# Kernel optimization log

Hardware: AMD Instinct MI355X
Metric: run time of the kernel (lower is better)

The kernel has to match this reference:

```python
import jax, jax.numpy as jnp
import numpy as np
from jax import lax

B, T, C, H, K = 2, 4096, 2048, 16, 4
D = C // H
EPS = 1e-5


def _ln(x, g, b):
    m = x.mean(-1, keepdims=True)
    v = ((x - m) ** 2).mean(-1, keepdims=True)
    return (x - m) / jnp.sqrt(v + EPS) * g + b


def _l2norm(x):
    n = jnp.sqrt(jnp.sum(x * x, axis=-1, keepdims=True))
    return x / jnp.maximum(n, 1e-12)


def setup_inputs() -> dict:
    key = jax.random.key(0)
    ks = jax.random.split(key, 10)
    s = 1.0 / np.sqrt(C)
    x = jax.random.normal(ks[0], (B, T, C), jnp.float32)
    Wq = jax.random.normal(ks[1], (C, C), jnp.float32) * s
    Wk = jax.random.normal(ks[2], (C, C), jnp.float32) * s
    Wv = jax.random.normal(ks[3], (C, C), jnp.float32) * s
    Wo = jax.random.normal(ks[4], (C, C), jnp.float32) * s
    conv_w = jax.random.normal(ks[5], (C, 1, K), jnp.float32) * 0.5  # depthwise (O, I/g, K)
    conv_b = jnp.zeros((C,), jnp.float32)
    Wig = jax.random.normal(ks[6], (C, C), jnp.float32) * 0.02
    big = jnp.full((C,), -2.0, jnp.float32)  # gate_init_bias
    Wog = jax.random.normal(ks[7], (C, C), jnp.float32) * s
    bog = jnp.zeros((C,), jnp.float32)
    Wgam = jax.random.normal(ks[8], (H, C), jnp.float32) * 0.02
    decays = 1.0 - np.exp(np.linspace(np.log(1 - 0.9), np.log(1 - 0.9999), H))
    bgam = jnp.asarray(np.log(decays / (1 - decays)), jnp.float32)
    vn_g = jnp.ones((D,), jnp.float32); vn_b = jnp.zeros((D,), jnp.float32)
    mn_g = jnp.ones((D,), jnp.float32); mn_b = jnp.zeros((D,), jnp.float32)
    gn_g = jnp.ones((C,), jnp.float32); gn_b = jnp.zeros((C,), jnp.float32)
    return dict(x=x, Wq=Wq, Wk=Wk, Wv=Wv, Wo=Wo, conv_w=conv_w, conv_b=conv_b,
                Wig=Wig, big=big, Wog=Wog, bog=bog, Wgam=Wgam, bgam=bgam,
                vn_g=vn_g, vn_b=vn_b, mn_g=mn_g, mn_b=mn_b, gn_g=gn_g, gn_b=gn_b)


def reference(x, Wq, Wk, Wv, Wo, conv_w, conv_b, Wig, big, Wog, bog, Wgam, bgam,
              vn_g, vn_b, mn_g, mn_b, gn_g, gn_b):
    # Causal depthwise conv1d over time
    xt = jnp.transpose(x, (0, 2, 1))                     # [B,C,T]
    xp = jnp.pad(xt, ((0, 0), (0, 0), (K - 1, 0)))
    xc = lax.conv_general_dilated(xp, conv_w, (1,), 'VALID', feature_group_count=C)
    xc = xc + conv_b[None, :, None]
    x_conv = jax.nn.silu(jnp.transpose(xc, (0, 2, 1)))   # [B,T,C]

    q = _l2norm((x @ Wq.T).reshape(B, T, H, D))
    k = _l2norm((x @ Wk.T).reshape(B, T, H, D))
    v = _ln((x @ Wv.T).reshape(B, T, H, D), vn_g, vn_b)
    i_gate = jax.nn.sigmoid(x_conv @ Wig.T + big).reshape(B, T, H, D)
    gamma = jax.nn.sigmoid(x_conv @ Wgam.T + bgam).reshape(B, T, H, 1)

    # Gated linear recurrence: mem_t = gamma_t * mem_{t-1} + i_t * k_t * v_t
    kv = i_gate * k * v
    def combine(c1, c2):
        a1, b1 = c1
        a2, b2 = c2
        return a1 * a2, a2 * b1 + b2
    _, mem = lax.associative_scan(combine, (gamma, kv), axis=1)  # mem: [B,T,H,D]

    mem_out = _ln(mem, mn_g, mn_b)
    out = (mem_out * q).reshape(B * T, H, D)
    # GroupNorm(num_groups=H) over channels
    m = out.mean(-1, keepdims=True)
    var = ((out - m) ** 2).mean(-1, keepdims=True)
    out = (out - m) / jnp.sqrt(var + EPS)
    out = out * gn_g.reshape(H, D) + gn_b.reshape(H, D)
    out = out.reshape(B, T, C)
    out = out * jax.nn.sigmoid(x_conv @ Wog.T + bog)
    return out @ Wo.T
```

## Files before the change

### kernel.cpp

```cpp
#include <hip/hip_runtime.h>
#include <cstdint>
#include <cstddef>

using u16 = unsigned short;
using bf16x8 = __attribute__((ext_vector_type(8))) __bf16;
using f32x4  = __attribute__((ext_vector_type(4))) float;

constexpr int Bb = 2, Tt = 4096, Cc = 2048, Hh = 16, Dd = 128;
constexpr int Mm = Bb * Tt;
constexpr int CHK = 32;
constexpr int NCH = Tt / CHK;
constexpr float EPSf = 1e-5f;

__device__ __forceinline__ u16 f2bf(float f) {
  union { float f; uint32_t u; } v; v.f = f;
  return (u16)((v.u + 0x7fffu + ((v.u >> 16) & 1u)) >> 16);
}
__device__ __forceinline__ float bf2f(u16 h) {
  union { uint32_t u; float f; } v; v.u = ((uint32_t)h) << 16;
  return v.f;
}
__device__ __forceinline__ float sig_(float z) { return 1.f / (1.f + __expf(-z)); }
__device__ __forceinline__ float wred(float v) {
#pragma unroll
  for (int m = 32; m; m >>= 1) v += __shfl_xor(v, m);
  return v;
}
__device__ __forceinline__ void glds16(const u16* g, u16* l) {
  __builtin_amdgcn_global_load_lds(
      (const __attribute__((address_space(1))) unsigned int*)g,
      (__attribute__((address_space(3))) unsigned int*)l, 16, 0, 0);
}

__global__ void la_conv(const float* __restrict__ x, const float* __restrict__ cw,
                        const float* __restrict__ cb, u16* __restrict__ xbf,
                        u16* __restrict__ xconv) {
  int i4 = blockIdx.x * 256 + threadIdx.x;
  int c4 = i4 & (Cc / 4 - 1);
  int bt = i4 >> 9;
  int t = bt & (Tt - 1);
  const float4* x4 = (const float4*)x;
  float4 xv = x4[i4];
  float4 xm1 = t >= 1 ? x4[i4 - Cc / 4] : make_float4(0, 0, 0, 0);
  float4 xm2 = t >= 2 ? x4[i4 - Cc / 2] : make_float4(0, 0, 0, 0);
  float4 xm3 = t >= 3 ? x4[i4 - 3 * Cc / 4] : make_float4(0, 0, 0, 0);
  ushort4 ob; ushort4 oc;
  const float4* cw4 = (const float4*)cw;
  float vv[4]  = {xv.x, xv.y, xv.z, xv.w};
  float v1[4]  = {xm1.x, xm1.y, xm1.z, xm1.w};
  float v2[4]  = {xm2.x, xm2.y, xm2.z, xm2.w};
  float v3[4]  = {xm3.x, xm3.y, xm3.z, xm3.w};
  u16 rb[4], rc[4];
#pragma unroll
  for (int j = 0; j < 4; j++) {
    int c = c4 * 4 + j;
    float4 w = cw4[c];
    float acc = cb[c] + w.w * vv[j] + w.z * v1[j] + w.y * v2[j] + w.x * v3[j];
    rb[j] = f2bf(vv[j]);
    rc[j] = f2bf(acc * sig_(acc));
  }
  ob.x = rb[0]; ob.y = rb[1]; ob.z = rb[2]; ob.w = rb[3];
  oc.x = rc[0]; oc.y = rc[1]; oc.z = rc[2]; oc.w = rc[3];
  ((ushort4*)xbf)[i4] = ob;
  ((ushort4*)xconv)[i4] = oc;
}

__global__ void la_cvt5(const float* w0, const float* w1, const float* w2,
                        const float* w3, const float* w4,
                        u16* o0, u16* o1, u16* o2, u16* o3, u16* o4, int n4each) {
  int i = blockIdx.x * 256 + threadIdx.x;
  int seg = i / n4each;
  int off = i - seg * n4each;
  const float* src = seg == 0 ? w0 : seg == 1 ? w1 : seg == 2 ? w2 : seg == 3 ? w3 : w4;
  u16* dst = seg == 0 ? o0 : seg == 1 ? o1 : seg == 2 ? o2 : seg == 3 ? o3 : o4;
  float4 v = ((const float4*)src)[off];
  ushort4 o;
  o.x = f2bf(v.x); o.y = f2bf(v.y); o.z = f2bf(v.z); o.w = f2bf(v.w);
  ((ushort4*)dst)[off] = o;
}

__global__ void la_cvt(const float* __restrict__ in, u16* __restrict__ out, int n4) {
  int i = blockIdx.x * 256 + threadIdx.x;
  if (i < n4) {
    float4 v = ((const float4*)in)[i];
    ushort4 o;
    o.x = f2bf(v.x); o.y = f2bf(v.y); o.z = f2bf(v.z); o.w = f2bf(v.w);
    ((ushort4*)out)[i] = o;
  }
}

__global__ __launch_bounds__(256) void la_gamma(
    const u16* __restrict__ xconv, const float* __restrict__ Wg,
    const float* __restrict__ bg, float* __restrict__ gam) {
  __shared__ u16 wlds[Hh * Cc];
  for (int i = threadIdx.x; i < Hh * Cc / 4; i += 256) {
    float4 v = ((const float4*)Wg)[i];
    ushort4 o;
    o.x = f2bf(v.x); o.y = f2bf(v.y); o.z = f2bf(v.z); o.w = f2bf(v.w);
    ((ushort4*)wlds)[i] = o;
  }
  __syncthreads();
  const int wave = threadIdx.x >> 6, lane = threadIdx.x & 63;
  const int row0 = blockIdx.x * 16 + wave * 4;
#pragma unroll
  for (int r = 0; r < 4; r++) {
    const int row = row0 + r;
    const u16* xr = xconv + (size_t)row * Cc + lane * 8;
    bf16x8 xv[4];
#pragma unroll
    for (int it = 0; it < 4; it++) xv[it] = *(const bf16x8*)(xr + it * 512);
#pragma unroll
    for (int h = 0; h < 16; h++) {
      const u16* wr = wlds + h * Cc + lane * 8;
      float acc = 0.f;
#pragma unroll
      for (int it = 0; it < 4; it++) {
        bf16x8 wv = *(const bf16x8*)(wr + it * 512);
#pragma unroll
        for (int e = 0; e < 8; e++) acc += (float)xv[it][e] * (float)wv[e];
      }
      acc = wred(acc);
      if (lane == 0) gam[row * Hh + h] = sig_(acc + bg[h]);
    }
  }
}

__global__ void la_prep(const u16* pq, const u16* pk, const u16* pv, const u16* pig,
                        const float* __restrict__ vng, const float* __restrict__ vnb,
                        const float* __restrict__ bigv, u16* qo, u16* kvo) {
  const int wave = threadIdx.x >> 6, lane = threadIdx.x & 63;
  const int p = blockIdx.x * 4 + wave;
  const int row = p >> 4, h = p & 15;
  const int d0 = lane * 2;
  const size_t base = (size_t)row * Cc + h * Dd + d0;
  uint32_t uq = *(const uint32_t*)(pq + base);
  uint32_t uk = *(const uint32_t*)(pk + base);
  uint32_t uv = *(const uint32_t*)(pv + base);
  uint32_t ui = *(const uint32_t*)(pig + base);
  float q0 = bf2f((u16)uq), q1 = bf2f((u16)(uq >> 16));
  float k0 = bf2f((u16)uk), k1 = bf2f((u16)(uk >> 16));
  float v0 = bf2f((u16)uv), v1 = bf2f((u16)(uv >> 16));
  float i0 = bf2f((u16)ui), i1 = bf2f((u16)(ui >> 16));
  float qs = wred(q0*q0 + q1*q1);
  float ks = wred(k0*k0 + k1*k1);
  float s1 = wred(v0 + v1);
  float s2 = wred(v0*v0 + v1*v1);
  float qn = 1.f / fmaxf(sqrtf(qs), 1e-12f);
  float kn = 1.f / fmaxf(sqrtf(ks), 1e-12f);
  float mu = s1 * (1.f / Dd);
  float var = s2 * (1.f / Dd) - mu * mu;
  float rs = rsqrtf(var + EPSf);
  int c0 = h * Dd + d0;
  float vh0 = (v0 - mu) * rs * vng[d0]     + vnb[d0];
  float vh1 = (v1 - mu) * rs * vng[d0 + 1] + vnb[d0 + 1];
  float ig0 = sig_(i0 + bigv[c0]);
  float ig1 = sig_(i1 + bigv[c0 + 1]);
  float kv0 = ig0 * (k0 * kn) * vh0;
  float kv1 = ig1 * (k1 * kn) * vh1;
  *(uint32_t*)(qo + base)  = (uint32_t)f2bf(q0 * qn) | ((uint32_t)f2bf(q1 * qn) << 16);
  *(uint32_t*)(kvo + base) = (uint32_t)f2bf(kv0)     | ((uint32_t)f2bf(kv1) << 16);
}

__global__ void la_scan1(u16* __restrict__ kv, float* __restrict__ gam,
                         float* __restrict__ Ebuf) {
  const int wave = threadIdx.x >> 6, lane = threadIdx.x & 63;
  const int p = blockIdx.x * 4 + wave;
  const int bh = p >> 7, c = p & (NCH - 1);
  const int b = bh >> 4, h = bh & 15;
  const int t0 = c * CHK;
  const size_t rbase = (size_t)b * Tt + t0;
  const size_t base = rbase * Cc + h * Dd + lane * 2;
  float* gp = gam + rbase * Hh + h;
  float m0 = 0.f, m1 = 0.f, cg = 1.f;
#pragma unroll 4
  for (int t = 0; t < CHK; t++) {
    float g = gp[(size_t)t * Hh];
    cg *= g;
    uint32_t u = *(const uint32_t*)(kv + base + (size_t)t * Cc);
    m0 = fmaf(g, m0, bf2f((u16)u));
    m1 = fmaf(g, m1, bf2f((u16)(u >> 16)));
    *(uint32_t*)(kv + base + (size_t)t * Cc) =
        (uint32_t)f2bf(m0) | ((uint32_t)f2bf(m1) << 16);
    if (lane == 0) gp[(size_t)t * Hh] = cg;
  }
  float2 e; e.x = m0; e.y = m1;
  *(float2*)&Ebuf[(size_t)p * Dd + lane * 2] = e;
}

__global__ void la_scan2(const float* __restrict__ Ebuf, const float* __restrict__ cumg,
                         float* __restrict__ carry) {
  const int bh = blockIdx.x;
  const int b = bh >> 4, h = bh & 15;
  const int lane = threadIdx.x;
  float S0 = 0.f, S1 = 0.f;
  for (int c = 0; c < NCH; c++) {
    size_t idx = ((size_t)bh * NCH + c) * Dd + lane * 2;
    float2 s; s.x = S0; s.y = S1;
    *(float2*)&carry[idx] = s;
    float2 E = *(const float2*)&Ebuf[idx];
    float P = cumg[((size_t)b * Tt + c * CHK + CHK - 1) * Hh + h];
    S0 = fmaf(P, S0, E.x);
    S1 = fmaf(P, S1, E.y);
  }
}

__global__ void la_post(const u16* mem, const u16* q, const u16* ogp,
                        const float* __restrict__ cumg, const float* __restrict__ carry,
                        const float* __restrict__ mng, const float* __restrict__ mnb,
                        const float* __restrict__ gng, const float* __restrict__ gnb,
                        const float* __restrict__ bog, u16* outb) {
  const int wave = threadIdx.x >> 6, lane = threadIdx.x & 63;
  const int p = blockIdx.x * 4 + wave;
  const int row = p >> 4, h = p & 15;
  const int b = row >> 12, t = row & (Tt - 1), ch = t >> 5;
  const int d0 = lane * 2;
  const size_t base = (size_t)row * Cc + h * Dd + d0;
  uint32_t um = *(const uint32_t*)(mem + base);
  uint32_t uq = *(const uint32_t*)(q + base);
  uint32_t uo = *(const uint32_t*)(ogp + base);
  float cg = cumg[p];
  float2 cr = *(const float2*)&carry[(((size_t)(b * Hh + h)) * NCH + ch) * Dd + d0];
  float m0 = fmaf(cg, cr.x, bf2f((u16)um));
  float m1 = fmaf(cg, cr.y, bf2f((u16)(um >> 16)));
  float q0 = bf2f((u16)uq), q1 = bf2f((u16)(uq >> 16));
  float g0 = bf2f((u16)uo), g1 = bf2f((u16)(uo >> 16));
  float s1 = wred(m0 + m1);
  float s2 = wred(m0*m0 + m1*m1);
  float mu = s1 * (1.f / Dd);
  float var = s2 * (1.f / Dd) - mu * mu;
  float rs = rsqrtf(var + EPSf);
  int c0 = h * Dd + d0;
  float mo0 = (m0 - mu) * rs * mng[d0]     + mnb[d0];
  float mo1 = (m1 - mu) * rs * mng[d0 + 1] + mnb[d0 + 1];
  float o0 = mo0 * q0, o1 = mo1 * q1;
  float t1 = wred(o0 + o1);
  float t2 = wred(o0*o0 + o1*o1);
  float mu2 = t1 * (1.f / Dd);
  float var2 = t2 * (1.f / Dd) - mu2 * mu2;
  float rs2 = rsqrtf(var2 + EPSf);
  float y0 = (o0 - mu2) * rs2 * gng[c0]     + gnb[c0];
  float y1 = (o1 - mu2) * rs2 * gng[c0 + 1] + gnb[c0 + 1];
  y0 *= sig_(g0 + bog[c0]);
  y1 *= sig_(g1 + bog[c0 + 1]);
  *(uint32_t*)(outb + base) = (uint32_t)f2bf(y0) | ((uint32_t)f2bf(y1) << 16);
}

template <int OUT_BF16>
__global__ __launch_bounds__(256)
void la_gemm(const u16* __restrict__ A,
             const u16* __restrict__ W0, const u16* __restrict__ W1,
             const u16* __restrict__ W2,
             void* __restrict__ C0, void* __restrict__ C1, void* __restrict__ C2,
             int K) {
  __shared__ u16 As[128 * 64];
  __shared__ u16 Bs[128 * 64];
  const int tid = threadIdx.x;
  const int lane = tid & 63;
  const int wave = tid >> 6;
  const int seg = blockIdx.x >> 4;
  const int bn = (blockIdx.x & 15) * 128;
  const int bm = blockIdx.y * 128;
  const u16* W = seg == 0 ? W0 : (seg == 1 ? W1 : W2);
  void* Co = seg == 0 ? C0 : (seg == 1 ? C1 : C2);
  const int wm = (wave >> 1) * 64;
  const int wn = (wave & 1) * 64;
  const int fm = lane & 15;

  const int srow = wave * 32 + (lane >> 3);
  const int sg   = ((lane & 7) ^ (lane >> 3)) * 8;
  const u16* Ag = A + (size_t)(bm + srow) * K + sg;
  const u16* Wg = W + (size_t)(bn + srow) * K + sg;
  u16* lA = As + wave * 2048;
  u16* lB = Bs + wave * 2048;

  f32x4 acc[4][4] = {};

  for (int k0 = 0; k0 < K; k0 += 64) {
#pragma unroll
    for (int j = 0; j < 4; j++) {
      glds16(Ag + k0 + j * 8 * K, lA + j * 512);
      glds16(Wg + k0 + j * 8 * K, lB + j * 512);
    }
    __syncthreads();
#pragma unroll
    for (int kk = 0; kk < 2; kk++) {
      const int qs = (((lane >> 4) + kk * 4) ^ (fm & 7)) * 8;
      bf16x8 af[4], bfr[4];
#pragma unroll
      for (int i = 0; i < 4; i++)
        af[i] = *(const bf16x8*)&As[(wm + i * 16 + fm) * 64 + qs];
#pragma unroll
      for (int j = 0; j < 4; j++)
        bfr[j] = *(const bf16x8*)&Bs[(wn + j * 16 + fm) * 64 + qs];
#pragma unroll
      for (int i = 0; i < 4; i++)
#pragma unroll
        for (int j = 0; j < 4; j++)
          acc[i][j] = __builtin_amdgcn_mfma_f32_16x16x32_bf16(af[i], bfr[j], acc[i][j], 0, 0, 0);
    }
    __syncthreads();
  }

  const int cr = (lane >> 4) * 4;
  const int cc = lane & 15;
#pragma unroll
  for (int i = 0; i < 4; i++) {
#pragma unroll
    for (int j = 0; j < 4; j++) {
#pragma unroll
      for (int r = 0; r < 4; r++) {
        size_t off = (size_t)(bm + wm + i * 16 + cr + r) * Cc + (bn + wn + j * 16 + cc);
        if (OUT_BF16) ((u16*)Co)[off] = f2bf(acc[i][j][r]);
        else          ((float*)Co)[off] = acc[i][j][r];
      }
    }
  }
}

extern "C" void kernel_launch(void* const* d_in, const int* in_sizes, int n_in,
                              void* d_out, int out_size, void* d_ws, size_t ws_size,
                              hipStream_t stream) {
  (void)in_sizes; (void)n_in; (void)out_size; (void)ws_size;
  const float* x    = (const float*)d_in[0];
  const float* Wq   = (const float*)d_in[1];
  const float* Wk   = (const float*)d_in[2];
  const float* Wv   = (const float*)d_in[3];
  const float* Wo   = (const float*)d_in[4];
  const float* cw   = (const float*)d_in[5];
  const float* cb   = (const float*)d_in[6];
  const float* Wig  = (const float*)d_in[7];
  const float* big  = (const float*)d_in[8];
  const float* Wog  = (const float*)d_in[9];
  const float* bog  = (const float*)d_in[10];
  const float* Wgam = (const float*)d_in[11];
  const float* bgam = (const float*)d_in[12];
  const float* vng  = (const float*)d_in[13];
  const float* vnb  = (const float*)d_in[14];
  const float* mng  = (const float*)d_in[15];
  const float* mnb  = (const float*)d_in[16];
  const float* gng  = (const float*)d_in[17];
  const float* gnb  = (const float*)d_in[18];

  char* ws = (char*)d_ws;
  const size_t NB = (size_t)Mm * Cc * 2;
  u16* xbf   = (u16*)(ws + 0 * NB);
  u16* xconv = (u16*)(ws + 1 * NB);
  u16* preq  = (u16*)(ws + 2 * NB);
  u16* prek  = (u16*)(ws + 3 * NB);
  u16* prev  = (u16*)(ws + 4 * NB);
  u16* preig = (u16*)(ws + 5 * NB);
  u16* wbf   = (u16*)(ws + 6 * NB);
  float* gam = (float*)(ws + 6 * NB + (size_t)Cc * Cc * 2);
  const size_t WE = (size_t)Cc * Cc;
  u16* wk_bf  = preig;
  u16* wv_bf  = preig + WE;
  u16* wig_bf = preig + 2 * WE;
  u16* wog_bf = preig + 3 * WE;
  float* Ebuf  = (float*)preig;
  float* carry = (float*)(preig + 1024 * 1024);
  u16* ogscr = (u16*)d_out;

  const int WN4 = Cc * Cc / 4;
  dim3 blk(256);

  la_conv<<<Mm * Cc / 4 / 256, blk, 0, stream>>>(x, cw, cb, xbf, xconv);

  la_cvt5<<<5 * WN4 / 256, blk, 0, stream>>>(Wq, Wk, Wv, Wig, Wog,
                                             wbf, wk_bf, wv_bf, wig_bf, wog_bf, WN4);

  la_gemm<1><<<dim3(48, Mm / 128), blk, 0, stream>>>(
      xbf, wbf, wk_bf, wv_bf, (void*)preq, (void*)prek, (void*)prev, Cc);

  la_cvt<<<WN4 / 256, blk, 0, stream>>>(Wo, wbf, WN4);

  la_gemm<1><<<dim3(32, Mm / 128), blk, 0, stream>>>(
      xconv, wig_bf, wog_bf, wog_bf, (void*)xbf, (void*)ogscr, (void*)ogscr, Cc);

  la_gamma<<<Mm / 16, blk, 0, stream>>>(xconv, Wgam, bgam, gam);

  la_prep<<<Mm * Hh / 4, blk, 0, stream>>>(preq, prek, prev, xbf,
                                           vng, vnb, big, preq, prek);

  la_scan1<<<Bb * Hh * NCH / 4, blk, 0, stream>>>(prek, gam, Ebuf);
  la_scan2<<<Bb * Hh, dim3(64), 0, stream>>>(Ebuf, gam, carry);

  la_post<<<Mm * Hh / 4, blk, 0, stream>>>(prek, preq, ogscr, gam, carry,
                                           mng, mnb, gng, gnb, bog, xbf);

  la_gemm<0><<<dim3(16, Mm / 128), blk, 0, stream>>>(
      xbf, wbf, wbf, wbf, d_out, d_out, d_out, Cc);
}
```

Measured before the change: 855.2 us.

## Rewrite bf16 GEMM as 256x256 tile with 8 waves and double-buffered LDS pipeline

Replaces the 128x128, 4-wave GEMM with a 256x256 tile computed by 8 waves. The tile is split into four 128-row/128-col sub-blocks, and global-to-LDS loads are staged two iterations ahead in a double-buffered 128KB LDS region, with raw s_barrier and explicit waitcnt interleaving loads and MFMAs. It raises per-block data reuse and hides memory latency behind MFMA work. The cost is a much larger LDS footprint and register pressure, and the hand-placed barriers and vmcnt counts are fragile.

```diff
diff --git a/kernel.cpp b/kernel.cpp
--- a/kernel.cpp
+++ b/kernel.cpp
@@ -31,6 +31,7 @@
       (const __attribute__((address_space(1))) unsigned int*)g,
       (__attribute__((address_space(3))) unsigned int*)l, 16, 0, 0);
 }
+__device__ __forceinline__ void bar_() { asm volatile("s_barrier" ::: "memory"); }
 
 __global__ void la_conv(const float* __restrict__ x, const float* __restrict__ cw,
                         const float* __restrict__ cb, u16* __restrict__ xbf,
@@ -245,76 +246,129 @@
   *(uint32_t*)(outb + base) = (uint32_t)f2bf(y0) | ((uint32_t)f2bf(y1) << 16);
 }
 
+#define STAGE(t, j) do {                                                        \
+    const u16* _s = (((j) == 0 || (j) == 2) ? Ab : Wb)                          \
+                    + (((j) == 1 || (j) == 2) ? (size_t)128 * K : (size_t)0)    \
+                    + soff + (size_t)(t) * 64;                                  \
+    u16* _d = dbase + ((((t) & 1) * 4 + (j)) * 8192);                           \
+    glds16(_s, _d);                                                             \
+    glds16(_s + 8 * (size_t)K, _d + 512);                                       \
+  } while (0)
+
+#define LDFRAG(DST, NFR, SLOT, RBASE) do {                                      \
+    _Pragma("unroll")                                                           \
+    for (int _i = 0; _i < (NFR); ++_i)                                          \
+      _Pragma("unroll")                                                         \
+      for (int _ks = 0; _ks < 2; ++_ks)                                         \
+        DST[_i][_ks] = *(const bf16x8*)&(SLOT)[((RBASE) + _i * 16) * 64 +       \
+                         ((((lane >> 4) + _ks * 4) ^ x7) * 8)];                 \
+  } while (0)
+
+#define MM16(QM, QN, BB) do {                                                   \
+    __builtin_amdgcn_s_setprio(1);                                             \
+    _Pragma("unroll")                                                           \
+    for (int _mi = 0; _mi < 4; ++_mi)                                           \
+      _Pragma("unroll")                                                         \
+      for (int _ni = 0; _ni < 2; ++_ni)                                         \
+        _Pragma("unroll")                                                       \
+        for (int _ks = 0; _ks < 2; ++_ks)                                       \
+          acc[QM][QN][_mi][_ni] = __builtin_amdgcn_mfma_f32_16x16x32_bf16(      \
+              a[_mi][_ks], BB[_ni][_ks], acc[QM][QN][_mi][_ni], 0, 0, 0);       \
+    __builtin_amdgcn_s_setprio(0);                                             \
+  } while (0)
+
 template <int OUT_BF16>
-__global__ __launch_bounds__(256)
+__global__ __launch_bounds__(512, 2)
 void la_gemm(const u16* __restrict__ A,
              const u16* __restrict__ W0, const u16* __restrict__ W1,
              const u16* __restrict__ W2,
              void* __restrict__ C0, void* __restrict__ C1, void* __restrict__ C2,
              int K) {
-  __shared__ u16 As[128 * 64];
-  __shared__ u16 Bs[128 * 64];
-  const int tid = threadIdx.x;
+  __shared__ u16 lds[8 * 8192];
+  const int tid  = threadIdx.x;
   const int lane = tid & 63;
-  const int wave = tid >> 6;
-  const int seg = blockIdx.x >> 4;
-  const int bn = (blockIdx.x & 15) * 128;
-  const int bm = blockIdx.y * 128;
+  const int wv   = tid >> 6;
+  const int wm = wv >> 2;
+  const int wn = wv & 3;
+  const int fm = lane & 15;
+  const int x7 = fm & 7;
+  const int seg = blockIdx.x >> 3;
+  const int bn = (blockIdx.x & 7) * 256;
+  const int bm = blockIdx.y * 256;
   const u16* W = seg == 0 ? W0 : (seg == 1 ? W1 : W2);
   void* Co = seg == 0 ? C0 : (seg == 1 ? C1 : C2);
-  const int wm = (wave >> 1) * 64;
-  const int wn = (wave & 1) * 64;
-  const int fm = lane & 15;
-
-  const int srow = wave * 32 + (lane >> 3);
-  const int sg   = ((lane & 7) ^ (lane >> 3)) * 8;
-  const u16* Ag = A + (size_t)(bm + srow) * K + sg;
-  const u16* Wg = W + (size_t)(bn + srow) * K + sg;
-  u16* lA = As + wave * 2048;
-  u16* lB = Bs + wave * 2048;
-
-  f32x4 acc[4][4] = {};
-
-  for (int k0 = 0; k0 < K; k0 += 64) {
-#pragma unroll
-    for (int j = 0; j < 4; j++) {
-      glds16(Ag + k0 + j * 8 * K, lA + j * 512);
-      glds16(Wg + k0 + j * 8 * K, lB + j * 512);
-    }
-    __syncthreads();
-#pragma unroll
-    for (int kk = 0; kk < 2; kk++) {
-      const int qs = (((lane >> 4) + kk * 4) ^ (fm & 7)) * 8;
-      bf16x8 af[4], bfr[4];
-#pragma unroll
-      for (int i = 0; i < 4; i++)
-        af[i] = *(const bf16x8*)&As[(wm + i * 16 + fm) * 64 + qs];
-#pragma unroll
-      for (int j = 0; j < 4; j++)
-        bfr[j] = *(const bf16x8*)&Bs[(wn + j * 16 + fm) * 64 + qs];
-#pragma unroll
-      for (int i = 0; i < 4; i++)
-#pragma unroll
-        for (int j = 0; j < 4; j++)
-          acc[i][j] = __builtin_amdgcn_mfma_f32_16x16x32_bf16(af[i], bfr[j], acc[i][j], 0, 0, 0);
-    }
-    __syncthreads();
+
+  const u16* Ab = A + (size_t)bm * K;
+  const u16* Wb = W + (size_t)bn * K;
+  const size_t soff = (size_t)(wv * 16 + (lane >> 3)) * K
+                      + (size_t)(((lane & 7) ^ (lane >> 3)) * 8);
+  u16* const dbase = lds + wv * 1024;
+  const int nkt = K >> 6;
+  const int ra = wm * 64 + fm;
+  const int rb = wn * 32 + fm;
+
+  f32x4 acc[2][2][4][2] = {};
+  bf16x8 a[4][2], b0[2][2], b1[2][2];
+
+  STAGE(0, 0); STAGE(0, 1); STAGE(0, 2); STAGE(0, 3);
+  STAGE(1, 0); STAGE(1, 1); STAGE(1, 2);
+  asm volatile("s_waitcnt vmcnt(6)" ::: "memory");
+  bar_();
+
+  for (int kt = 0; kt < nkt; ++kt) {
+    const int b = kt & 1;
+    const u16* sA0 = lds + (b * 4 + 0) * 8192;
+    const u16* sB1 = lds + (b * 4 + 1) * 8192;
+    const u16* sA1 = lds + (b * 4 + 2) * 8192;
+    const u16* sB0 = lds + (b * 4 + 3) * 8192;
+
+    LDFRAG(a, 4, sA0, ra);
+    LDFRAG(b0, 2, sB0, rb);
+    if (kt + 1 < nkt) STAGE(kt + 1, 3);
+    bar_();
+    asm volatile("s_waitcnt lgkmcnt(0)" ::: "memory");
+    MM16(0, 0, b0);
+    bar_();
+
+    LDFRAG(b1, 2, sB1, rb);
+    if (kt + 2 < nkt) STAGE(kt + 2, 0);
+    bar_();
+    asm volatile("s_waitcnt lgkmcnt(0)" ::: "memory");
+    MM16(0, 1, b1);
+    bar_();
+
+    LDFRAG(a, 4, sA1, ra);
+    if (kt + 2 < nkt) STAGE(kt + 2, 1);
+    bar_();
+    asm volatile("s_waitcnt lgkmcnt(0)" ::: "memory");
+    MM16(1, 1, b1);
+    bar_();
+
+    if (kt + 2 < nkt) STAGE(kt + 2, 2);
+    bar_();
+    MM16(1, 0, b0);
+    if (kt < nkt - 2)       asm volatile("s_waitcnt vmcnt(6)" ::: "memory");
+    else if (kt == nkt - 2) asm volatile("s_waitcnt vmcnt(0)" ::: "memory");
+    bar_();
   }
 
   const int cr = (lane >> 4) * 4;
   const int cc = lane & 15;
 #pragma unroll
-  for (int i = 0; i < 4; i++) {
-#pragma unroll
-    for (int j = 0; j < 4; j++) {
-#pragma unroll
-      for (int r = 0; r < 4; r++) {
-        size_t off = (size_t)(bm + wm + i * 16 + cr + r) * Cc + (bn + wn + j * 16 + cc);
-        if (OUT_BF16) ((u16*)Co)[off] = f2bf(acc[i][j][r]);
-        else          ((float*)Co)[off] = acc[i][j][r];
-      }
-    }
-  }
+  for (int qm = 0; qm < 2; ++qm)
+#pragma unroll
+    for (int qn = 0; qn < 2; ++qn)
+#pragma unroll
+      for (int mi = 0; mi < 4; ++mi)
+#pragma unroll
+        for (int ni = 0; ni < 2; ++ni)
+#pragma unroll
+          for (int r = 0; r < 4; ++r) {
+            size_t off = (size_t)(bm + qm * 128 + wm * 64 + mi * 16 + cr + r) * Cc
+                         + (bn + qn * 128 + wn * 32 + ni * 16 + cc);
+            if (OUT_BF16) ((u16*)Co)[off] = f2bf(acc[qm][qn][mi][ni][r]);
+            else          ((float*)Co)[off] = acc[qm][qn][mi][ni][r];
+          }
 }
 
 extern "C" void kernel_launch(void* const* d_in, const int* in_sizes, int n_in,
@@ -362,18 +416,19 @@
 
   const int WN4 = Cc * Cc / 4;
   dim3 blk(256);
+  dim3 gblk(512);
 
   la_conv<<<Mm * Cc / 4 / 256, blk, 0, stream>>>(x, cw, cb, xbf, xconv);
 
   la_cvt5<<<5 * WN4 / 256, blk, 0, stream>>>(Wq, Wk, Wv, Wig, Wog,
                                              wbf, wk_bf, wv_bf, wig_bf, wog_bf, WN4);
 
-  la_gemm<1><<<dim3(48, Mm / 128), blk, 0, stream>>>(
+  la_gemm<1><<<dim3(24, Mm / 256), gblk, 0, stream>>>(
       xbf, wbf, wk_bf, wv_bf, (void*)preq, (void*)prek, (void*)prev, Cc);
 
   la_cvt<<<WN4 / 256, blk, 0, stream>>>(Wo, wbf, WN4);
 
-  la_gemm<1><<<dim3(32, Mm / 128), blk, 0, stream>>>(
+  la_gemm<1><<<dim3(16, Mm / 256), gblk, 0, stream>>>(
       xconv, wig_bf, wog_bf, wog_bf, (void*)xbf, (void*)ogscr, (void*)ogscr, Cc);
 
   la_gamma<<<Mm / 16, blk, 0, stream>>>(xconv, Wgam, bgam, gam);
@@ -387,6 +442,6 @@
   la_post<<<Mm * Hh / 4, blk, 0, stream>>>(prek, preq, ogscr, gam, carry,
                                            mng, mnb, gng, gnb, bog, xbf);
 
-  la_gemm<0><<<dim3(16, Mm / 128), blk, 0, stream>>>(
+  la_gemm<0><<<dim3(8, Mm / 256), gblk, 0, stream>>>(
       xbf, wbf, wbf, wbf, d_out, d_out, d_out, Cc);
 }
```

Result: faster. 765.6 us (-10.5%).
